# Optimization experiments

Hardware: AMD Instinct MI355X
Metric: run time of the kernel (lower is better)

The kernel has to match this reference:

```python
import jax, jax.numpy as jnp
import numpy as np

B, S, D, H = 2, 2048, 1024, 16
HD = D // H
SCALE = HD ** -0.5
NEG = -1e30


def setup_inputs() -> dict:
    key = jax.random.key(0)
    ks = jax.random.split(key, 10)
    w = lambda k: jax.random.normal(k, (D, D), dtype=jnp.float32) * 0.02
    b = lambda k: jax.random.normal(k, (D,), dtype=jnp.float32) * 0.01
    hidden_states = jax.random.normal(ks[0], (B, S, D), dtype=jnp.float32)
    document_ids = jnp.sort(jax.random.randint(ks[1], (S,), 0, 16))
    return {
        'hidden_states': hidden_states,
        'wq': w(ks[2]), 'bq': b(ks[3]),
        'wk': w(ks[4]), 'bk': b(ks[5]),
        'wv': w(ks[6]), 'bv': b(ks[7]),
        'wo': w(ks[8]), 'bo': b(ks[9]),
        'document_ids': document_ids,
    }


def reference(hidden_states, wq, bq, wk, bk, wv, bv, wo, bo, document_ids):
    # projections (nn.Linear: x @ W.T + b)
    q = (hidden_states @ wq.T + bq).reshape(B, S, H, HD)
    k = (hidden_states @ wk.T + bk).reshape(B, S, H, HD)
    v = (hidden_states @ wv.T + bv).reshape(B, S, H, HD)
    # document-block mask: attend only within same document
    mask = document_ids[:, None] == document_ids[None, :]  # [S, S]
    scores = jnp.einsum('bqhd,bkhd->bhqk', q, k) * SCALE
    scores = jnp.where(mask[None, None], scores, NEG)
    attn = jax.nn.softmax(scores, axis=-1)
    out = jnp.einsum('bhqk,bkhd->bqhd', attn, v).reshape(B, S, D)
    return out @ wo.T + bo
```

## Files before the change

kernel.cpp:

```cpp
#include <hip/hip_runtime.h>
#include <hip/hip_bf16.h>
#include <math.h>

#define B 2
#define S 2048
#define D 1024
#define H 16
#define HD 64
#define SCALE 0.125f
#define NEGBIG -1e30f

#define NE 4194304
#define NW 1048576
#define NE8 524288
#define NW8 131072

typedef _Float16 f16;
typedef _Float16 f16x8 __attribute__((ext_vector_type(8)));
typedef _Float16 f16x4 __attribute__((ext_vector_type(4)));
typedef float f32x4  __attribute__((ext_vector_type(4)));

__device__ __forceinline__ void gl_lds16(const void* g, void* l) {
    __builtin_amdgcn_global_load_lds(
        (const __attribute__((address_space(1))) unsigned int*)g,
        (__attribute__((address_space(3))) unsigned int*)l, 16, 0, 0);
}

__device__ __forceinline__ void wave_lds_fence() {
    __builtin_amdgcn_wave_barrier();
    __builtin_amdgcn_s_waitcnt(0xC07F);
    __builtin_amdgcn_wave_barrier();
}

__global__ __launch_bounds__(256) void prep_k(
    const float4* __restrict__ hs,
    const float4* __restrict__ wq, const float4* __restrict__ wk,
    const float4* __restrict__ wv, const float4* __restrict__ wo,
    const int* __restrict__ doc,
    f16x8* __restrict__ xh, f16x8* __restrict__ wqkv, f16x8* __restrict__ woh,
    int* __restrict__ dstart, int* __restrict__ dend)
{
    int i = blockIdx.x * blockDim.x + threadIdx.x;
    if (i < NE8 + 4 * NW8) {
        const float4* src;
        f16x8* dst;
        if (i < NE8) { src = hs + 2 * (size_t)i; dst = xh + i; }
        else {
            int j = i - NE8;
            int id = j / NW8, jj = j - id * NW8;
            src = ((id == 0) ? wq : (id == 1) ? wk : (id == 2) ? wv : wo) + 2 * (size_t)jj;
            dst = (id < 3) ? (wqkv + (size_t)id * NW8 + jj) : (woh + jj);
        }
        float4 a = src[0], b = src[1];
        f16x8 h;
        h[0] = (f16)a.x; h[1] = (f16)a.y; h[2] = (f16)a.z; h[3] = (f16)a.w;
        h[4] = (f16)b.x; h[5] = (f16)b.y; h[6] = (f16)b.z; h[7] = (f16)b.w;
        *dst = h;
    } else {
        int s = i - (NE8 + 4 * NW8);
        if (s < S) {
            int v = doc[s];
            int lo = 0, hi = S;
            while (lo < hi) { int mid = (lo + hi) >> 1; if (doc[mid] < v) lo = mid + 1; else hi = mid; }
            dstart[s] = lo;
            lo = 0; hi = S;
            while (lo < hi) { int mid = (lo + hi) >> 1; if (doc[mid] <= v) lo = mid + 1; else hi = mid; }
            dend[s] = lo;
        }
    }
}

__global__ __launch_bounds__(512, 2) void qkv_mfma_k(
    const f16* __restrict__ xh, const f16* __restrict__ wqkv,
    const float* __restrict__ bq, const float* __restrict__ bk,
    const float* __restrict__ bv,
    f16* __restrict__ Qh, f16* __restrict__ Kh, f16* __restrict__ Vth)
{
    __shared__ union {
        struct { f16 At[2][256 * 64]; f16 Bt[2][256 * 64]; } s;
        f16 tr[64 * 264];
    } lds;

    const int l = blockIdx.x;
    const int swz = (l & 7) * 24 + (l >> 3);
    const int which = swz >> 6;
    const int r2 = swz & 63;
    const int m0 = (r2 >> 2) * 256, n0 = (r2 & 3) * 256;
    const f16* Bg = wqkv + (size_t)which * D * D;

    const int tid = threadIdx.x;
    const int w = tid >> 6, ln = tid & 63;
    const int wm = (w & 1) * 128, wn = (w >> 1) * 64;
    const int lc = ln & 15, quad = ln >> 4;

    const int srow = w * 8 + (ln >> 3);
    const int soct = (ln & 7) ^ (srow & 7);
    const size_t aBase = (size_t)(m0 + srow) * 1024 + soct * 8;
    const size_t bBase = (size_t)(n0 + srow) * 1024 + soct * 8;
    const int lBase = w * 512;

#define UA(u, kt, buf) gl_lds16(xh + aBase + (size_t)(u) * 65536 + (kt) * 64, lds.s.At[buf] + (u) * 4096 + lBase)
#define UB(u, kt, buf) gl_lds16(Bg + bBase + (size_t)(u) * 65536 + (kt) * 64, lds.s.Bt[buf] + (u) * 4096 + lBase)

    f32x4 acc[8][4];
    #pragma unroll
    for (int i = 0; i < 8; i++)
        #pragma unroll
        for (int j = 0; j < 4; j++) acc[i][j] = (f32x4){0.f, 0.f, 0.f, 0.f};

    UB(0, 0, 0); UB(1, 0, 0); UB(2, 0, 0); UB(3, 0, 0);
    UA(0, 0, 0); UA(1, 0, 0); UA(2, 0, 0); UA(3, 0, 0);
    UB(0, 1, 1); UB(1, 1, 1); UB(2, 1, 1); UA(0, 1, 1); UB(3, 1, 1); UA(2, 1, 1);
    asm volatile("s_waitcnt vmcnt(6)");
    __builtin_amdgcn_sched_barrier(0);
    __builtin_amdgcn_s_barrier();
    __builtin_amdgcn_sched_barrier(0);

#define READ_AF(q_, Ab_) { \
    _Pragma("unroll") \
    for (int tt = 0; tt < 2; tt++) { \
        int am = wm + ((q_) * 2 + tt) * 16 + lc; \
        _Pragma("unroll") \
        for (int ks = 0; ks < 2; ks++) \
            af[tt][ks] = *(const f16x8*)&Ab_[am * 64 + (((ks * 4 + quad) ^ (am & 7)) * 8)]; \
    } }

#define MFMA_Q(q_) { \
    __builtin_amdgcn_s_setprio(1); \
    _Pragma("unroll") \
    for (int ks = 0; ks < 2; ks++) \
        _Pragma("unroll") \
        for (int mt = 0; mt < 2; mt++) \
            _Pragma("unroll") \
            for (int nt = 0; nt < 4; nt++) \
                acc[(q_) * 2 + mt][nt] = __builtin_amdgcn_mfma_f32_16x16x32_f16( \
                    af[mt][ks], bf[nt][ks], acc[(q_) * 2 + mt][nt], 0, 0, 0); \
    __builtin_amdgcn_s_setprio(0); }

#define BAR_IN() { \
    __builtin_amdgcn_sched_barrier(0); \
    __builtin_amdgcn_s_barrier(); \
    asm volatile("s_waitcnt lgkmcnt(0)"); \
    __builtin_amdgcn_sched_barrier(0); }

#define BAR_OUT() { \
    __builtin_amdgcn_sched_barrier(0); \
    __builtin_amdgcn_s_barrier(); \
    __builtin_amdgcn_sched_barrier(0); }

    #pragma unroll 1
    for (int t = 0; t < 16; ++t) {
        const int cur = t & 1, nxt = cur ^ 1;
        const f16* Ab = lds.s.At[cur];
        const f16* Bb = lds.s.Bt[cur];
        f16x8 af[2][2], bf[4][2];

        #pragma unroll
        for (int nt = 0; nt < 4; nt++) {
            int bn = wn + nt * 16 + lc;
            #pragma unroll
            for (int ks = 0; ks < 2; ks++)
                bf[nt][ks] = *(const f16x8*)&Bb[bn * 64 + (((ks * 4 + quad) ^ (bn & 7)) * 8)];
        }
        READ_AF(0, Ab)
        if (t < 15) { UA(1, t + 1, nxt); UA(3, t + 1, nxt); }
        BAR_IN(); MFMA_Q(0); BAR_OUT();

        READ_AF(1, Ab)
        if (t < 14) { UB(0, t + 2, cur); UB(1, t + 2, cur); }
        BAR_IN(); MFMA_Q(1); BAR_OUT();

        READ_AF(2, Ab)
        if (t < 14) { UB(2, t + 2, cur); UA(0, t + 2, cur); }
        BAR_IN(); MFMA_Q(2); BAR_OUT();

        READ_AF(3, Ab)
        if (t < 14) { UB(3, t + 2, cur); UA(2, t + 2, cur); }
        BAR_IN(); MFMA_Q(3);
        if (t < 14)       { asm volatile("s_waitcnt vmcnt(6)"); }
        else if (t == 14) { asm volatile("s_waitcnt vmcnt(0)"); }
        BAR_OUT();
    }
#undef UA
#undef UB
#undef READ_AF
#undef MFMA_Q
#undef BAR_IN
#undef BAR_OUT

    if (which < 2) {
        const float* bias = (which == 0) ? bq : bk;
        f16* dst = (which == 0) ? Qh : Kh;
        #pragma unroll
        for (int nt = 0; nt < 4; nt++) {
            int col = n0 + wn + nt * 16 + lc;
            float bias_v = bias[col];
            int h = col >> 6, hd = col & 63;
            #pragma unroll
            for (int mt = 0; mt < 8; mt++) {
                #pragma unroll
                for (int r = 0; r < 4; r++) {
                    int m = m0 + wm + mt * 16 + quad * 4 + r;
                    int bbm = m >> 11, s = m & (S - 1);
                    float val = acc[mt][nt][r] + bias_v;
                    if (which == 0) val *= SCALE;
                    size_t idx = (((size_t)(bbm * H + h) * S) + s) * HD + hd;
                    dst[idx] = (f16)val;
                }
            }
        }
    } else {
        const int bb = m0 >> 11;
        const int sbase = m0 & (S - 1);
        __syncthreads();
        #pragma unroll
        for (int pass = 0; pass < 4; pass++) {
            if ((w >> 1) == pass) {
                #pragma unroll
                for (int nt = 0; nt < 4; nt++) {
                    int colp = nt * 16 + lc;
                    float bvv = bv[n0 + pass * 64 + colp];
                    #pragma unroll
                    for (int mt = 0; mt < 8; mt++) {
                        f16x4 v;
                        #pragma unroll
                        for (int r = 0; r < 4; r++) v[r] = (f16)(acc[mt][nt][r] + bvv);
                        *(f16x4*)&lds.tr[colp * 264 + wm + mt * 16 + quad * 4] = v;
                    }
                }
            }
            __syncthreads();
            #pragma unroll
            for (int p2 = 0; p2 < 4; p2++) {
                int chunk = tid + p2 * 512;
                int colp = chunk >> 5;
                int oct = chunk & 31;
                f16x8 v = *(const f16x8*)&lds.tr[colp * 264 + oct * 8];
                int vcol = n0 + pass * 64 + colp;
                int h = vcol >> 6, hd = vcol & 63;
                size_t idx = (((size_t)(bb * H + h) * HD) + hd) * S + sbase + oct * 8;
                *(f16x8*)(Vth + idx) = v;
            }
            __syncthreads();
        }
    }
}

__global__ __launch_bounds__(256) void out_mfma_k(
    const f16* __restrict__ oh, const f16* __restrict__ wh,
    const float* __restrict__ bias, float* __restrict__ Y)
{
    __shared__ f16 Ah[128 * 64], Bh[64 * 64];
    const int tid = threadIdx.x;
    const int w = tid >> 6, ln = tid & 63;
    const int wm = (w & 1) * 64, wn = (w >> 1) * 32;
    const int lc = ln & 15, quad = ln >> 4;
    const int m0 = blockIdx.y * 128, n0 = blockIdx.x * 64;

    f32x4 acc[4][2];
    #pragma unroll
    for (int i = 0; i < 4; i++)
        #pragma unroll
        for (int j = 0; j < 2; j++) acc[i][j] = (f32x4){0.f, 0.f, 0.f, 0.f};

    for (int k0 = 0; k0 < 1024; k0 += 64) {
        #pragma unroll
        for (int i = 0; i < 4; i++) {
            int rl = w * 32 + i * 8 + (ln >> 3);
            int oc = (ln & 7) ^ (rl & 7);
            gl_lds16(oh + (size_t)(m0 + rl) * 1024 + k0 + oc * 8, Ah + (w * 32 + i * 8) * 64);
        }
        #pragma unroll
        for (int i = 0; i < 2; i++) {
            int rl = w * 16 + i * 8 + (ln >> 3);
            int oc = (ln & 7) ^ (rl & 7);
            gl_lds16(wh + (size_t)(n0 + rl) * 1024 + k0 + oc * 8, Bh + (w * 16 + i * 8) * 64);
        }
        __syncthreads();

        #pragma unroll
        for (int ks = 0; ks < 2; ks++) {
            f16x8 ah[4], bh[2];
            #pragma unroll
            for (int t = 0; t < 4; t++) {
                int am = wm + t * 16 + lc;
                ah[t] = *(const f16x8*)&Ah[am * 64 + (((ks * 4 + quad) ^ (am & 7)) * 8)];
            }
            #pragma unroll
            for (int t = 0; t < 2; t++) {
                int bn = wn + t * 16 + lc;
                bh[t] = *(const f16x8*)&Bh[bn * 64 + (((ks * 4 + quad) ^ (bn & 7)) * 8)];
            }
            #pragma unroll
            for (int mt = 0; mt < 4; mt++)
                #pragma unroll
                for (int nt = 0; nt < 2; nt++)
                    acc[mt][nt] = __builtin_amdgcn_mfma_f32_16x16x32_f16(ah[mt], bh[nt], acc[mt][nt], 0, 0, 0);
        }
        __syncthreads();
    }

    #pragma unroll
    for (int nt = 0; nt < 2; nt++) {
        int col = n0 + wn + nt * 16 + lc;
        float bv_ = bias[col];
        #pragma unroll
        for (int mt = 0; mt < 4; mt++) {
            #pragma unroll
            for (int r = 0; r < 4; r++) {
                int m = m0 + wm + mt * 16 + quad * 4 + r;
                Y[(size_t)m * D + col] = acc[mt][nt][r] + bv_;
            }
        }
    }
}

__device__ __forceinline__ void load_kfrag(
    const f16* __restrict__ Kh, size_t bh, int j0, int lc, int quad, f16x8 kf[4][2])
{
    #pragma unroll
    for (int t = 0; t < 4; t++) {
        size_t krow = (bh + j0 + t * 16 + lc) * HD;
        #pragma unroll
        for (int ks = 0; ks < 2; ks++)
            kf[t][ks] = *(const f16x8*)(Kh + krow + ks * 32 + quad * 8);
    }
}

__global__ __launch_bounds__(256) void attn4_k(
    const f16* __restrict__ Qh, const f16* __restrict__ Kh,
    const f16* __restrict__ Vth,
    const int* __restrict__ dstart, const int* __restrict__ dend,
    f16* __restrict__ Ohi)
{
    const int qt = blockIdx.x, h = blockIdx.y, b = blockIdx.z;
    const int tid = threadIdx.x;
    const int w = tid >> 6, ln = tid & 63;
    const int lc = ln & 15, quad = ln >> 4;
    const int q0 = qt * 64 + w * 16;
    const size_t bh  = ((size_t)b * H + h) * S;
    const size_t bhv = ((size_t)b * H + h) * HD;

    __shared__ float Ps[4][2][16 * 65];

    int row_st[4], row_en[4];
    #pragma unroll
    for (int r = 0; r < 4; r++) {
        row_st[r] = dstart[q0 + quad * 4 + r];
        row_en[r] = dend[q0 + quad * 4 + r];
    }
    const int kstart = dstart[q0] & ~63;
    const int kend   = dend[q0 + 15];

    const size_t qrow = bh + q0 + lc;
    f16x8 qf[2];
    #pragma unroll
    for (int ks = 0; ks < 2; ks++)
        qf[ks] = *(const f16x8*)(Qh + qrow * HD + ks * 32 + quad * 8);

    f32x4 o[4];
    #pragma unroll
    for (int nt = 0; nt < 4; nt++) o[nt] = (f32x4){0.f, 0.f, 0.f, 0.f};
    f32x4 m_i = (f32x4){NEGBIG, NEGBIG, NEGBIG, NEGBIG};
    f32x4 l_i = (f32x4){0.f, 0.f, 0.f, 0.f};

    f16x8 kf[4][2], kf2[4][2];
    load_kfrag(Kh, bh, kstart, lc, quad, kf);

    int it = 0;
    for (int j0 = kstart; j0 < kend; j0 += 64, it ^= 1) {
        float* ps = &Ps[w][it][0];
        const bool more = (j0 + 64) < kend;
        if (more) load_kfrag(Kh, bh, j0 + 64, lc, quad, kf2);

        f32x4 sc[4];
        #pragma unroll
        for (int t = 0; t < 4; t++) {
            f32x4 a = (f32x4){0.f, 0.f, 0.f, 0.f};
            #pragma unroll
            for (int ks = 0; ks < 2; ks++)
                a = __builtin_amdgcn_mfma_f32_16x16x32_f16(qf[ks], kf[t][ks], a, 0, 0, 0);
            int key = j0 + t * 16 + lc;
            #pragma unroll
            for (int r = 0; r < 4; r++) {
                bool valid = (key >= row_st[r]) && (key < row_en[r]);
                sc[t][r] = valid ? a[r] : NEGBIG;
            }
        }

        f32x4 mx = sc[0];
        #pragma unroll
        for (int t = 1; t < 4; t++)
            #pragma unroll
            for (int r = 0; r < 4; r++) mx[r] = fmaxf(mx[r], sc[t][r]);
        #pragma unroll
        for (int off = 1; off <= 8; off <<= 1)
            #pragma unroll
            for (int r = 0; r < 4; r++) mx[r] = fmaxf(mx[r], __shfl_xor(mx[r], off, 64));

        f32x4 m_new, alpha;
        #pragma unroll
        for (int r = 0; r < 4; r++) {
            m_new[r] = fmaxf(m_i[r], mx[r]);
            alpha[r] = __expf(m_i[r] - m_new[r]);
        }

        f32x4 psum = (f32x4){0.f, 0.f, 0.f, 0.f};
        f32x4 pv[4];
        #pragma unroll
        for (int t = 0; t < 4; t++) {
            #pragma unroll
            for (int r = 0; r < 4; r++) {
                float p = __expf(sc[t][r] - m_new[r]);
                p = (sc[t][r] < -5e29f) ? 0.f : p;
                pv[t][r] = p;
                psum[r] += p;
            }
        }
        #pragma unroll
        for (int off = 1; off <= 8; off <<= 1)
            #pragma unroll
            for (int r = 0; r < 4; r++) psum[r] += __shfl_xor(psum[r], off, 64);

        #pragma unroll
        for (int r = 0; r < 4; r++) {
            l_i[r] = l_i[r] * alpha[r] + psum[r];
            m_i[r] = m_new[r];
        }
        #pragma unroll
        for (int nt = 0; nt < 4; nt++)
            #pragma unroll
            for (int r = 0; r < 4; r++) o[nt][r] *= alpha[r];

        f16x8 vh[2][4];
        #pragma unroll
        for (int ks = 0; ks < 2; ks++) {
            int gp = ks * 4 + quad;
            #pragma unroll
            for (int nt = 0; nt < 4; nt++) {
                int dim = nt * 16 + lc;
                vh[ks][nt] = *(const f16x8*)(Vth + (bhv + dim) * S + j0 + gp * 8);
            }
        }

        #pragma unroll
        for (int t = 0; t < 4; t++) {
            int g = 2 * t + (lc >> 3);
            #pragma unroll
            for (int r = 0; r < 4; r++) {
                int q = quad * 4 + r;
                ps[q * 65 + ((g ^ (q & 7)) * 8) + (lc & 7)] = pv[t][r];
            }
        }

        wave_lds_fence();

        #pragma unroll
        for (int ks = 0; ks < 2; ks++) {
            int gp = ks * 4 + quad;
            const float* prow = &ps[lc * 65 + ((gp ^ (lc & 7)) * 8)];
            f16x8 ph;
            #pragma unroll
            for (int j = 0; j < 8; j++) ph[j] = (f16)prow[j];
            #pragma unroll
            for (int nt = 0; nt < 4; nt++)
                o[nt] = __builtin_amdgcn_mfma_f32_16x16x32_f16(ph, vh[ks][nt], o[nt], 0, 0, 0);
        }

        if (more) {
            #pragma unroll
            for (int t = 0; t < 4; t++)
                #pragma unroll
                for (int ks = 0; ks < 2; ks++) kf[t][ks] = kf2[t][ks];
        }
    }

    f32x4 inv;
    #pragma unroll
    for (int r = 0; r < 4; r++) inv[r] = 1.f / l_i[r];
    #pragma unroll
    for (int nt = 0; nt < 4; nt++) {
        int dim = nt * 16 + lc;
        #pragma unroll
        for (int r = 0; r < 4; r++) {
            int q = q0 + quad * 4 + r;
            float val = o[nt][r] * inv[r];
            size_t idx = ((size_t)(b * S + q)) * D + h * 64 + dim;
            Ohi[idx] = (f16)val;
        }
    }
}

extern "C" void kernel_launch(void* const* d_in, const int* in_sizes, int n_in,
                              void* d_out, int out_size, void* d_ws, size_t ws_size,
                              hipStream_t stream) {
    const float* hs = (const float*)d_in[0];
    const float* wq = (const float*)d_in[1];
    const float* bq = (const float*)d_in[2];
    const float* wk = (const float*)d_in[3];
    const float* bk = (const float*)d_in[4];
    const float* wv = (const float*)d_in[5];
    const float* bv = (const float*)d_in[6];
    const float* wo = (const float*)d_in[7];
    const float* bo = (const float*)d_in[8];
    const int*  doc = (const int*)d_in[9];
    float* out = (float*)d_out;

    f16* xh   = (f16*)d_ws;
    f16* Qhb  = xh + NE;
    f16* Khb  = Qhb + NE;
    f16* Vth  = Khb + NE;
    f16* wqkv = Vth + NE;
    f16* woh  = wqkv + 3 * (size_t)NW;
    int* dstart = (int*)(woh + NW);
    int* dend = dstart + S;

    prep_k<<<(NE8 + 4 * NW8 + S + 255) / 256, 256, 0, stream>>>(
        (const float4*)hs, (const float4*)wq, (const float4*)wk,
        (const float4*)wv, (const float4*)wo, doc,
        (f16x8*)xh, (f16x8*)wqkv, (f16x8*)woh, dstart, dend);

    qkv_mfma_k<<<192, 512, 0, stream>>>(
        xh, wqkv, bq, bk, bv, Qhb, Khb, Vth);
    attn4_k<<<dim3(S / 64, H, B), 256, 0, stream>>>(
        Qhb, Khb, Vth, dstart, dend, xh);
    out_mfma_k<<<dim3(D / 64, (B * S) / 128), 256, 0, stream>>>(xh, woh, bo, out);
}
```

Baseline: 183.2 us.

## Double-buffer output projection GEMM loads and drop QKV block swizzle

The output projection kernel now uses two LDS buffers with async global-to-LDS loads issued two stages ahead, manual vmcnt waits and raw barriers, so tile loads overlap the MFMA compute. Address offsets are hoisted out of the k-loop, and MFMA issue is wrapped in raised wave priority. Separately, the QKV GEMM drops its XCD-aware block index swizzle in favour of a plain 3D grid, which may change L2 locality across chiplets. Doubling LDS in the output kernel may reduce occupancy.

```diff
diff --git a/kernel.cpp b/kernel.cpp
--- a/kernel.cpp
+++ b/kernel.cpp
@@ -81,11 +81,8 @@
         f16 tr[64 * 264];
     } lds;
 
-    const int l = blockIdx.x;
-    const int swz = (l & 7) * 24 + (l >> 3);
-    const int which = swz >> 6;
-    const int r2 = swz & 63;
-    const int m0 = (r2 >> 2) * 256, n0 = (r2 & 3) * 256;
+    const int which = blockIdx.z;
+    const int m0 = blockIdx.y * 256, n0 = blockIdx.x * 256;
     const f16* Bg = wqkv + (size_t)which * D * D;
 
     const int tid = threadIdx.x;
@@ -250,33 +247,54 @@
     const f16* __restrict__ oh, const f16* __restrict__ wh,
     const float* __restrict__ bias, float* __restrict__ Y)
 {
-    __shared__ f16 Ah[128 * 64], Bh[64 * 64];
+    __shared__ f16 Ah[2][128 * 64];
+    __shared__ f16 Bh[2][64 * 64];
     const int tid = threadIdx.x;
     const int w = tid >> 6, ln = tid & 63;
     const int wm = (w & 1) * 64, wn = (w >> 1) * 32;
     const int lc = ln & 15, quad = ln >> 4;
     const int m0 = blockIdx.y * 128, n0 = blockIdx.x * 64;
 
+    size_t aoff[4], boff[2];
+    int lA[4], lB[2];
+    #pragma unroll
+    for (int i = 0; i < 4; i++) {
+        int rl = w * 32 + i * 8 + (ln >> 3);
+        int oc = (ln & 7) ^ (rl & 7);
+        aoff[i] = (size_t)(m0 + rl) * 1024 + oc * 8;
+        lA[i] = (w * 32 + i * 8) * 64;
+    }
+    #pragma unroll
+    for (int i = 0; i < 2; i++) {
+        int rl = w * 16 + i * 8 + (ln >> 3);
+        int oc = (ln & 7) ^ (rl & 7);
+        boff[i] = (size_t)(n0 + rl) * 1024 + oc * 8;
+        lB[i] = (w * 16 + i * 8) * 64;
+    }
+
     f32x4 acc[4][2];
     #pragma unroll
     for (int i = 0; i < 4; i++)
         #pragma unroll
         for (int j = 0; j < 2; j++) acc[i][j] = (f32x4){0.f, 0.f, 0.f, 0.f};
 
-    for (int k0 = 0; k0 < 1024; k0 += 64) {
-        #pragma unroll
-        for (int i = 0; i < 4; i++) {
-            int rl = w * 32 + i * 8 + (ln >> 3);
-            int oc = (ln & 7) ^ (rl & 7);
-            gl_lds16(oh + (size_t)(m0 + rl) * 1024 + k0 + oc * 8, Ah + (w * 32 + i * 8) * 64);
-        }
-        #pragma unroll
-        for (int i = 0; i < 2; i++) {
-            int rl = w * 16 + i * 8 + (ln >> 3);
-            int oc = (ln & 7) ^ (rl & 7);
-            gl_lds16(wh + (size_t)(n0 + rl) * 1024 + k0 + oc * 8, Bh + (w * 16 + i * 8) * 64);
-        }
-        __syncthreads();
+    #define OSTAGE(buf, k0) { \
+        _Pragma("unroll") \
+        for (int i_ = 0; i_ < 4; i_++) gl_lds16(oh + aoff[i_] + (k0), Ah[buf] + lA[i_]); \
+        _Pragma("unroll") \
+        for (int i_ = 0; i_ < 2; i_++) gl_lds16(wh + boff[i_] + (k0), Bh[buf] + lB[i_]); }
+
+    OSTAGE(0, 0)
+    OSTAGE(1, 64)
+    asm volatile("s_waitcnt vmcnt(6)");
+    __builtin_amdgcn_sched_barrier(0);
+    __builtin_amdgcn_s_barrier();
+    __builtin_amdgcn_sched_barrier(0);
+
+    for (int kt = 0; kt < 16; ++kt) {
+        const int cur = kt & 1;
+        const f16* Ac = Ah[cur];
+        const f16* Bc = Bh[cur];
 
         #pragma unroll
         for (int ks = 0; ks < 2; ks++) {
@@ -284,21 +302,37 @@
             #pragma unroll
             for (int t = 0; t < 4; t++) {
                 int am = wm + t * 16 + lc;
-                ah[t] = *(const f16x8*)&Ah[am * 64 + (((ks * 4 + quad) ^ (am & 7)) * 8)];
+                ah[t] = *(const f16x8*)&Ac[am * 64 + (((ks * 4 + quad) ^ (am & 7)) * 8)];
             }
             #pragma unroll
             for (int t = 0; t < 2; t++) {
                 int bn = wn + t * 16 + lc;
-                bh[t] = *(const f16x8*)&Bh[bn * 64 + (((ks * 4 + quad) ^ (bn & 7)) * 8)];
-            }
+                bh[t] = *(const f16x8*)&Bc[bn * 64 + (((ks * 4 + quad) ^ (bn & 7)) * 8)];
+            }
+            __builtin_amdgcn_s_setprio(1);
             #pragma unroll
             for (int mt = 0; mt < 4; mt++)
                 #pragma unroll
                 for (int nt = 0; nt < 2; nt++)
                     acc[mt][nt] = __builtin_amdgcn_mfma_f32_16x16x32_f16(ah[mt], bh[nt], acc[mt][nt], 0, 0, 0);
-        }
-        __syncthreads();
-    }
+            __builtin_amdgcn_s_setprio(0);
+        }
+
+        if (kt == 15) break;
+
+        __builtin_amdgcn_s_barrier();
+        __builtin_amdgcn_sched_barrier(0);
+        if (kt + 2 < 16) {
+            OSTAGE(cur, (kt + 2) * 64)
+            asm volatile("s_waitcnt vmcnt(6)");
+        } else {
+            asm volatile("s_waitcnt vmcnt(0)");
+        }
+        __builtin_amdgcn_sched_barrier(0);
+        __builtin_amdgcn_s_barrier();
+        __builtin_amdgcn_sched_barrier(0);
+    }
+    #undef OSTAGE
 
     #pragma unroll
     for (int nt = 0; nt < 2; nt++) {
@@ -520,7 +554,7 @@
         (const float4*)wv, (const float4*)wo, doc,
         (f16x8*)xh, (f16x8*)wqkv, (f16x8*)woh, dstart, dend);
 
-    qkv_mfma_k<<<192, 512, 0, stream>>>(
+    qkv_mfma_k<<<dim3(D / 256, (B * S) / 256, 3), 512, 0, stream>>>(
         xh, wqkv, bq, bk, bv, Qhb, Khb, Vth);
     attn4_k<<<dim3(S / 64, H, B), 256, 0, stream>>>(
         Qhb, Khb, Vth, dstart, dend, xh);
```

After: 182.8 us. About the same (-0.2%).
